# Optimization experiments

Measured on AMD Instinct MI355X. Metric: run time of the kernel, lower is better.

Reference implementation:

```python
import jax, jax.numpy as jnp
import numpy as np

G = 16  # grid (window) size, fixed in the module


def _ln_channels(x, w, b, eps=1e-5):
    # LayerNorm4D: normalize over channel dim of NCHW
    mu = x.mean(axis=1, keepdims=True)
    var = ((x - mu) ** 2).mean(axis=1, keepdims=True)
    return (x - mu) / jnp.sqrt(var + eps) * w[None, :, None, None] + b[None, :, None, None]


def setup_inputs() -> dict:
    key = jax.random.key(0)
    ks = jax.random.split(key, 8)
    B, C, H, W = 8, 256, 128, 128
    C8, F = C // 8, 4 * C
    s = 0.02
    return {
        "x": jax.random.normal(ks[0], (B, C, H, W), jnp.float32),
        "Wq": jax.random.normal(ks[1], (C8, C), jnp.float32) * s,
        "Wk": jax.random.normal(ks[2], (C8, C), jnp.float32) * s,
        "Wv": jax.random.normal(ks[3], (C, C), jnp.float32) * s,
        "gamma": jnp.float32(1.0),
        "W1": jax.random.normal(ks[4], (F, C), jnp.float32) * s,
        "b1": jnp.zeros((F,), jnp.float32),
        "W2": jax.random.normal(ks[5], (C, F), jnp.float32) * s,
        "b2": jnp.zeros((C,), jnp.float32),
        "ln1_w": jnp.ones((C,), jnp.float32),
        "ln1_b": jnp.zeros((C,), jnp.float32),
        "ln2_w": jnp.ones((C,), jnp.float32),
        "ln2_b": jnp.zeros((C,), jnp.float32),
    }


def reference(x, Wq, Wk, Wv, gamma, W1, b1, W2, b2, ln1_w, ln1_b, ln2_w, ln2_b):
    B, C, H, W = x.shape
    nh, nw = H // G, W // G
    N = G * G  # tokens per window
    # gather all 16x16 windows into the batch dim: [B*nh*nw, C, N]
    xw = x.reshape(B, C, nh, G, nw, G).transpose(0, 2, 4, 1, 3, 5).reshape(B * nh * nw, C, N)
    # SAGAN-style self-attention within each window
    q = jnp.einsum('oc,bcn->bno', Wq, xw)                 # [Bw, N, C/8]
    k = jnp.einsum('oc,bcn->bon', Wk, xw)                 # [Bw, C/8, N]
    attn = jax.nn.softmax(jnp.einsum('bno,bom->bnm', q, k), axis=-1)  # [Bw, N, N]
    v = jnp.einsum('oc,bcn->bon', Wv, xw)                 # [Bw, C, N]
    out = jnp.einsum('bcn,bmn->bcm', v, attn)             # v @ attn^T
    aw = gamma * out + xw
    # scatter windows back to NCHW
    xa = aw.reshape(B, nh, nw, C, G, G).transpose(0, 3, 1, 4, 2, 5).reshape(B, C, H, W)
    # FFN: 1x1 conv -> GELU(exact) -> 1x1 conv (dropout is identity in eval)
    h1 = jax.nn.gelu(jnp.einsum('fc,bchw->bfhw', W1, xa) + b1[None, :, None, None], approximate=False)
    y = jnp.einsum('cf,bfhw->bchw', W2, h1) + b2[None, :, None, None]
    x2 = xa + _ln_channels(y, ln1_w, ln1_b)
    return x2 + _ln_channels(x2, ln2_w, ln2_b)
```

## Files before the change

### kernel.cpp

```cpp
#include <hip/hip_runtime.h>
#include <hip/hip_bf16.h>

#define C_DIM 256
#define HW_DIM 16384
#define F_DIM 1024

typedef __hip_bfloat16 bf16;
typedef short short8 __attribute__((ext_vector_type(8)));
typedef float f32x4 __attribute__((ext_vector_type(4)));

__device__ __forceinline__ float bf2f(unsigned short u) {
  unsigned int x = ((unsigned int)u) << 16;
  return __uint_as_float(x);
}
__device__ __forceinline__ unsigned short f2bfbits(float v) {
  bf16 h = __float2bfloat16(v);
  return *(unsigned short*)&h;
}


__global__ __launch_bounds__(256) void prep_weights(
    const float* __restrict__ Wq, const float* __restrict__ Wk,
    const float* __restrict__ Wv, const float* __restrict__ W1,
    const float* __restrict__ W2, unsigned short* __restrict__ Wqkv,
    unsigned short* __restrict__ W1s, unsigned short* __restrict__ W2s) {
  int i = blockIdx.x * 256 + threadIdx.x;
  if (i < 320 * 256) {
    int r = i >> 8, c = i & 255;
    float v;
    if (r < 32)      v = Wq[r * 256 + c];
    else if (r < 64) v = Wk[(r - 32) * 256 + c];
    else             v = Wv[(r - 64) * 256 + c];
    Wqkv[i] = f2bfbits(v);
  }
  if (i < 32768) {
    int ft = i >> 9, ks = (i >> 6) & 7, l = i & 63;
    int f = ft * 16 + (l & 15), kb = ks * 32 + (l >> 4) * 8;
    #pragma unroll
    for (int j = 0; j < 8; ++j)
      W1s[i * 8 + j] = f2bfbits(W1[f * 256 + kb + j]);
  }
  if (i < 32768) {
    int ct = i >> 11, gks = (i >> 6) & 31, l = i & 63;
    int c = ct * 16 + (l & 15), fb = gks * 32 + (l >> 4) * 8;
    #pragma unroll
    for (int j = 0; j < 8; ++j)
      W2s[i * 8 + j] = f2bfbits(W2[c * 1024 + fb + j]);
  }
}

__global__ __launch_bounds__(256) void qkvx_kernel(
    const float* __restrict__ x, const unsigned short* __restrict__ Wqkv,
    unsigned short* __restrict__ Xfrag, unsigned short* __restrict__ Qw,
    unsigned short* __restrict__ Kw, unsigned short* __restrict__ Vw) {
  __shared__ __align__(16) short Xs[4][8][64][8];

  const int bid = blockIdx.x;
  const int win = bid >> 2, mc = bid & 3;
  const int b = win >> 6, wh = (win >> 3) & 7, ww = win & 7;
  const int m0 = mc * 64;
  const int tid = threadIdx.x;
  const int wv = tid >> 6, l = tid & 63;
  const int t = l & 15, q = l >> 4;

  unsigned short* XFb = Xfrag + (size_t)win * 65536 + (size_t)mc * 16384;
  short8* XsLin = (short8*)&Xs[0][0][0][0];

  #pragma unroll
  for (int rep = 0; rep < 8; ++rep) {
    const int idx = rep * 256 + tid;
    const int mt_l = idx >> 9, kss = (idx >> 6) & 7, ll = idx & 63;
    const int tt = ll & 15, qq = ll >> 4;
    const int h = wh * 16 + mc * 4 + mt_l, w = ww * 16 + tt;
    const int c0 = kss * 32 + qq * 8;
    const float* xp = x + ((size_t)(b * 256 + c0) * 128 + h) * 128 + w;
    short8 v;
    #pragma unroll
    for (int j = 0; j < 8; ++j)
      v[j] = (short)f2bfbits(xp[(size_t)j * 16384]);
    XsLin[idx] = v;
    *(short8*)(XFb + (size_t)idx * 8) = v;
  }
  __syncthreads();

  const int r0 = wv * 16;
  unsigned short* const QKdst = (wv < 2) ? Qw : Kw;
  const int o0 = (wv & 1) * 16 + q * 4;

  for (int mt = 0; mt < 4; ++mt) {
    short8 Bf[8];
    #pragma unroll
    for (int ks = 0; ks < 8; ++ks)
      Bf[ks] = *(const short8*)&Xs[mt][ks][l][0];

    {
      f32x4 acc = (f32x4){0.f, 0.f, 0.f, 0.f};
      #pragma unroll
      for (int ks = 0; ks < 8; ++ks) {
        short8 av = *(const short8*)(Wqkv + (size_t)(r0 + t) * 256 + ks * 32 + q * 8);
        acc = __builtin_amdgcn_mfma_f32_16x16x32_bf16(av, Bf[ks], acc, 0, 0, 0);
      }
      const int n = m0 + mt * 16 + t;
      ushort4 u;
      u.x = f2bfbits(acc[0]); u.y = f2bfbits(acc[1]);
      u.z = f2bfbits(acc[2]); u.w = f2bfbits(acc[3]);
      *(ushort4*)(QKdst + ((size_t)win * 256 + n) * 32 + o0) = u;
    }

    #pragma unroll
    for (int i = 0; i < 4; ++i) {
      const int c0 = (wv * 4 + i) * 16;
      f32x4 acc = (f32x4){0.f, 0.f, 0.f, 0.f};
      #pragma unroll
      for (int ks = 0; ks < 8; ++ks) {
        short8 av = *(const short8*)(Wqkv + (size_t)(64 + c0 + t) * 256 + ks * 32 + q * 8);
        acc = __builtin_amdgcn_mfma_f32_16x16x32_bf16(Bf[ks], av, acc, 0, 0, 0);
      }
      ushort4 u;
      u.x = f2bfbits(acc[0]); u.y = f2bfbits(acc[1]);
      u.z = f2bfbits(acc[2]); u.w = f2bfbits(acc[3]);
      *(ushort4*)(Vw + ((size_t)win * 256 + c0 + t) * 256 + m0 + mt * 16 + q * 4) = u;
    }
  }
}

__global__ __launch_bounds__(256, 3) void attn_ffn_kernel(
    const unsigned short* __restrict__ Qw, const unsigned short* __restrict__ Kw,
    const unsigned short* __restrict__ Vw, const unsigned short* __restrict__ Xfrag,
    const float* __restrict__ gamma,
    const unsigned short* __restrict__ W1s, const unsigned short* __restrict__ W2s,
    const float* __restrict__ b1, const float* __restrict__ b2,
    const float* __restrict__ ln1w, const float* __restrict__ ln1b,
    const float* __restrict__ ln2w, const float* __restrict__ ln2b,
    float* __restrict__ out) {
  __shared__ __align__(16) short XfPs[16384];
  __shared__ __align__(16) short Htf[4][4][64][8];
  __shared__ float red[2][4][64];
  __shared__ float Ls[64];

  short (*Ps)[64][72] = (short(*)[64][72])&XfPs[0];
  float* Lpart = (float*)&XfPs[9216];
  short (*Xf)[8][64][8] = (short(*)[8][64][8])&XfPs[0];

  const int bid = blockIdx.x;
  const int wgb = (bid & 7) * 256 + (bid >> 3);
  const int win = wgb >> 2, wr = wgb & 3;
  const int b = win >> 6, wh = (win >> 3) & 7, ww = win & 7;

  const int tid = threadIdx.x;
  const int wc = tid >> 6, l = tid & 63;
  const int t = l & 15, q = l >> 4;

  f32x4 Oacc[4][4];
  #pragma unroll
  for (int k = 0; k < 4; ++k)
    #pragma unroll
    for (int i = 0; i < 4; ++i)
      Oacc[k][i] = (f32x4){0.f, 0.f, 0.f, 0.f};
  float lsum[16];
  #pragma unroll
  for (int e = 0; e < 16; ++e) lsum[e] = 0.f;

  const unsigned short* Qb = Qw + (size_t)win * 256 * 32;
  const unsigned short* Kb = Kw + (size_t)win * 256 * 32;
  const unsigned short* Vb = Vw + (size_t)win * 65536;

  short8 aq[4];
  #pragma unroll
  for (int i = 0; i < 4; ++i)
    aq[i] = *(const short8*)(Qb + (size_t)((wr * 4 + i) * 16 + t) * 32 + q * 8);

  for (int mcc = 0; mcc < 4; ++mcc) {
    const int buf = mcc & 1;
    {
      const int m0s = (mcc * 4 + wc) * 16;
      short8 bk = *(const short8*)(Kb + (size_t)(m0s + t) * 32 + q * 8);
      f32x4 sv[4];
      #pragma unroll
      for (int i = 0; i < 4; ++i)
        sv[i] = __builtin_amdgcn_mfma_f32_16x16x32_bf16(aq[i], bk, (f32x4){0.f,0.f,0.f,0.f}, 0, 0, 0);
      #pragma unroll
      for (int i = 0; i < 4; ++i) {
        #pragma unroll
        for (int r = 0; r < 4; ++r) {
          float e = __expf(sv[i][r]);
          lsum[i * 4 + r] += e;
          Ps[buf][i * 16 + q * 4 + r][wc * 16 + t] = (short)f2bfbits(e);
        }
      }
    }
    __syncthreads();
    #pragma unroll
    for (int ks2 = 0; ks2 < 2; ++ks2) {
      short8 ap[4], bv[4];
      #pragma unroll
      for (int i = 0; i < 4; ++i)
        ap[i] = *(const short8*)&Ps[buf][i * 16 + t][ks2 * 32 + q * 8];
      #pragma unroll
      for (int k = 0; k < 4; ++k)
        bv[k] = *(const short8*)(Vb + (size_t)((wc * 4 + k) * 16 + t) * 256 + mcc * 64 + ks2 * 32 + q * 8);
      #pragma unroll
      for (int k = 0; k < 4; ++k)
        #pragma unroll
        for (int i = 0; i < 4; ++i)
          Oacc[k][i] = __builtin_amdgcn_mfma_f32_16x16x32_bf16(bv[k], ap[i], Oacc[k][i], 0, 0, 0);
    }
  }

  #pragma unroll
  for (int mask = 1; mask < 16; mask <<= 1)
    #pragma unroll
    for (int e = 0; e < 16; ++e)
      lsum[e] += __shfl_xor(lsum[e], mask);
  __syncthreads();
  if (t == 0) {
    #pragma unroll
    for (int i = 0; i < 4; ++i)
      *(float4*)&Lpart[wc * 64 + i * 16 + q * 4] =
          make_float4(lsum[i * 4 + 0], lsum[i * 4 + 1], lsum[i * 4 + 2], lsum[i * 4 + 3]);
  }
  __syncthreads();
  if (tid < 64) {
    float s = Lpart[tid] + Lpart[64 + tid] + Lpart[128 + tid] + Lpart[192 + tid];
    Ls[tid] = gamma[0] / s;
  }
  __syncthreads();

  const unsigned short* Xres = Xfrag + (size_t)win * 65536;
  #pragma unroll
  for (int i = 0; i < 4; ++i) {
    const float ls = Ls[i * 16 + t];
    #pragma unroll
    for (int k = 0; k < 4; ++k) {
      const int ksx = wc * 2 + (k >> 1);
      const int lx = ((k & 1) * 2 + (q >> 1)) * 16 + t;
      const int jx = (q & 1) * 4;
      const size_t goff = (((size_t)(wr * 4 + i) * 8 + ksx) * 64 + lx) * 8 + jx;
      ushort4 xa4 = *(const ushort4*)(Xres + goff);
      const unsigned short* xp = (const unsigned short*)&xa4;
      ushort4 u;
      unsigned short* up = (unsigned short*)&u;
      #pragma unroll
      for (int r = 0; r < 4; ++r)
        up[r] = f2bfbits(ls * Oacc[k][i][r] + bf2f(xp[r]));
      *(ushort4*)&Xf[i][ksx][lx][jx] = u;
    }
  }
  __syncthreads();

  const int p = t;
  const int wv = wc;

  f32x4 Yacc[4][4];
  #pragma unroll
  for (int i = 0; i < 4; ++i)
    #pragma unroll
    for (int pt = 0; pt < 4; ++pt)
      Yacc[i][pt] = (f32x4){0.f, 0.f, 0.f, 0.f};

  const short8* W1s8 = (const short8*)W1s;
  const short8* W2s8 = (const short8*)W2s;

  for (int fc = 0; fc < 8; ++fc) {
    f32x4 Hacc[2][4];
    #pragma unroll
    for (int i = 0; i < 2; ++i)
      #pragma unroll
      for (int pt = 0; pt < 4; ++pt)
        Hacc[i][pt] = (f32x4){0.f, 0.f, 0.f, 0.f};
    const int f0 = (fc * 8 + wv * 2) * 8;
    #pragma unroll
    for (int ks = 0; ks < 8; ++ks) {
      short8 a0 = W1s8[(f0 + ks) * 64 + l];
      short8 a1 = W1s8[(f0 + 8 + ks) * 64 + l];
      #pragma unroll
      for (int pt = 0; pt < 4; ++pt) {
        short8 bf = *(const short8*)&Xf[pt][ks][l][0];
        Hacc[0][pt] = __builtin_amdgcn_mfma_f32_16x16x32_bf16(a0, bf, Hacc[0][pt], 0, 0, 0);
        Hacc[1][pt] = __builtin_amdgcn_mfma_f32_16x16x32_bf16(a1, bf, Hacc[1][pt], 0, 0, 0);
      }
    }
    __syncthreads();
    #pragma unroll
    for (int i = 0; i < 2; ++i) {
      float4 bv1 = *(const float4*)(b1 + fc * 128 + wv * 32 + i * 16 + q * 4);
      #pragma unroll
      for (int pt = 0; pt < 4; ++pt) {
        ushort4 hbv;
        unsigned short* hp = (unsigned short*)&hbv;
        #pragma unroll
        for (int r = 0; r < 4; ++r) {
          float v = Hacc[i][pt][r] + ((const float*)&bv1)[r];
          float a = 1.5957691216f * fmaf(0.044715f * v, v * v, v);
          float e = __expf(a);
          float g = v - v * __builtin_amdgcn_rcpf(e + 1.f);
          hp[r] = f2bfbits(g);
        }
        *(ushort4*)&Htf[pt][wv][(i * 2 + (q >> 1)) * 16 + p][(q & 1) * 4] = hbv;
      }
    }
    __syncthreads();
    #pragma unroll
    for (int fs = 0; fs < 4; ++fs) {
      short8 av[4];
      #pragma unroll
      for (int i = 0; i < 4; ++i)
        av[i] = W2s8[((wv * 4 + i) * 32 + fc * 4 + fs) * 64 + l];
      #pragma unroll
      for (int pt = 0; pt < 4; ++pt) {
        short8 bf = *(const short8*)&Htf[pt][fs][l][0];
        #pragma unroll
        for (int i = 0; i < 4; ++i)
          Yacc[i][pt] = __builtin_amdgcn_mfma_f32_16x16x32_bf16(av[i], bf, Yacc[i][pt], 0, 0, 0);
      }
    }
  }

  #pragma unroll
  for (int i = 0; i < 4; ++i) {
    float4 bb = *(const float4*)(b2 + wv * 64 + i * 16 + q * 4);
    #pragma unroll
    for (int pt = 0; pt < 4; ++pt)
      #pragma unroll
      for (int r = 0; r < 4; ++r)
        Yacc[i][pt][r] += ((const float*)&bb)[r];
  }

  #pragma unroll
  for (int pt = 0; pt < 4; ++pt) {
    float ss = 0.f, sq = 0.f;
    #pragma unroll
    for (int i = 0; i < 4; ++i)
      #pragma unroll
      for (int r = 0; r < 4; ++r) { float v = Yacc[i][pt][r]; ss += v; sq += v * v; }
    ss += __shfl_xor(ss, 16); sq += __shfl_xor(sq, 16);
    ss += __shfl_xor(ss, 32); sq += __shfl_xor(sq, 32);
    if (l < 16) { red[0][wv][pt * 16 + l] = ss; red[1][wv][pt * 16 + l] = sq; }
  }
  __syncthreads();
  if (tid < 64) {
    float S  = red[0][0][tid] + red[0][1][tid] + red[0][2][tid] + red[0][3][tid];
    float Q2 = red[1][0][tid] + red[1][1][tid] + red[1][2][tid] + red[1][3][tid];
    float m = S * 0.00390625f;
    float va = Q2 * 0.00390625f - m * m;
    red[0][0][tid] = m; red[1][0][tid] = rsqrtf(va + 1e-5f);
  }
  __syncthreads();
  #pragma unroll
  for (int i = 0; i < 4; ++i) {
    float4 w1v = *(const float4*)(ln1w + wv * 64 + i * 16 + q * 4);
    float4 b1v = *(const float4*)(ln1b + wv * 64 + i * 16 + q * 4);
    const int ksx = wv * 2 + (i >> 1);
    const int lq = (i & 1) * 2 + (q >> 1);
    #pragma unroll
    for (int pt = 0; pt < 4; ++pt) {
      int px = pt * 16 + p;
      float mu = red[0][0][px], rs = red[1][0][px];
      ushort4 xa4 = *(const ushort4*)&Xf[pt][ksx][lq * 16 + p][(q & 1) * 4];
      const unsigned short* xp = (const unsigned short*)&xa4;
      #pragma unroll
      for (int r = 0; r < 4; ++r)
        Yacc[i][pt][r] = bf2f(xp[r]) + (Yacc[i][pt][r] - mu) * rs * ((const float*)&w1v)[r] + ((const float*)&b1v)[r];
    }
  }
  __syncthreads();
  #pragma unroll
  for (int pt = 0; pt < 4; ++pt) {
    float ss = 0.f, sq = 0.f;
    #pragma unroll
    for (int i = 0; i < 4; ++i)
      #pragma unroll
      for (int r = 0; r < 4; ++r) { float v = Yacc[i][pt][r]; ss += v; sq += v * v; }
    ss += __shfl_xor(ss, 16); sq += __shfl_xor(sq, 16);
    ss += __shfl_xor(ss, 32); sq += __shfl_xor(sq, 32);
    if (l < 16) { red[0][wv][pt * 16 + l] = ss; red[1][wv][pt * 16 + l] = sq; }
  }
  __syncthreads();
  if (tid < 64) {
    float S  = red[0][0][tid] + red[0][1][tid] + red[0][2][tid] + red[0][3][tid];
    float Q2 = red[1][0][tid] + red[1][1][tid] + red[1][2][tid] + red[1][3][tid];
    float m = S * 0.00390625f;
    float va = Q2 * 0.00390625f - m * m;
    red[0][0][tid] = m; red[1][0][tid] = rsqrtf(va + 1e-5f);
  }
  __syncthreads();
  #pragma unroll
  for (int i = 0; i < 4; ++i) {
    float4 w2v = *(const float4*)(ln2w + wv * 64 + i * 16 + q * 4);
    float4 b2v = *(const float4*)(ln2b + wv * 64 + i * 16 + q * 4);
    #pragma unroll
    for (int pt = 0; pt < 4; ++pt) {
      int px = pt * 16 + p;
      float mu = red[0][0][px], rs = red[1][0][px];
      #pragma unroll
      for (int r = 0; r < 4; ++r) {
        int c = wv * 64 + i * 16 + q * 4 + r;
        float x2 = Yacc[i][pt][r];
        float o = x2 + (x2 - mu) * rs * ((const float*)&w2v)[r] + ((const float*)&b2v)[r];
        out[(((size_t)(b * 256 + c) * 128) + wh * 16 + wr * 4 + pt) * 128 + ww * 16 + p] = o;
      }
    }
  }
}

extern "C" void kernel_launch(void* const* d_in, const int* in_sizes, int n_in,
                              void* d_out, int out_size, void* d_ws, size_t ws_size,
                              hipStream_t stream) {
  const float* x     = (const float*)d_in[0];
  const float* Wq    = (const float*)d_in[1];
  const float* Wk    = (const float*)d_in[2];
  const float* Wv    = (const float*)d_in[3];
  const float* gamma = (const float*)d_in[4];
  const float* W1    = (const float*)d_in[5];
  const float* b1    = (const float*)d_in[6];
  const float* W2    = (const float*)d_in[7];
  const float* b2    = (const float*)d_in[8];
  const float* ln1w  = (const float*)d_in[9];
  const float* ln1b  = (const float*)d_in[10];
  const float* ln2w  = (const float*)d_in[11];
  const float* ln2b  = (const float*)d_in[12];
  float* out = (float*)d_out;

  char* wsb = (char*)d_ws;
  unsigned short* Xfrag = (unsigned short*)wsb;
  unsigned short* Vw    = (unsigned short*)(wsb + 67108864);
  unsigned short* Qw    = (unsigned short*)(wsb + 134217728);
  unsigned short* Kw    = (unsigned short*)(wsb + 142606336);
  unsigned short* Wqkv  = (unsigned short*)(wsb + 150994944);
  unsigned short* W1s   = (unsigned short*)(wsb + 151158784);
  unsigned short* W2s   = (unsigned short*)(wsb + 151683072);

  prep_weights<<<1024, 256, 0, stream>>>(Wq, Wk, Wv, W1, W2, Wqkv, W1s, W2s);
  qkvx_kernel<<<2048, 256, 0, stream>>>(x, Wqkv, Xfrag, Qw, Kw, Vw);
  attn_ffn_kernel<<<2048, 256, 0, stream>>>(Qw, Kw, Vw, Xfrag, gamma,
                                            W1s, W2s, b1, b2, ln1w, ln1b, ln2w, ln2b, out);
}
```

Before: 580.9 us.

## Coalesce x loads, hoist QKV weights, halve FFN tile for 4 waves/SIMD

The QKV projection kernel now reads x with float4 loads that are coalesced along width and scatters them into the LDS fragment layout. Xfrag is then copied out of LDS, and the weight fragments are hoisted out of the token loop. The attention+FFN kernel splits each FFN chunk into two halves with a smaller hidden tile and aliases the Ls/red buffers into one shared array, cutting LDS use and registers so occupancy can rise from 3 to 4 workgroups. The cost is twice as many barriers in the FFN loop and a risk of register spills under the tighter launch bound.

```diff
diff --git a/kernel.cpp b/kernel.cpp
--- a/kernel.cpp
+++ b/kernel.cpp
@@ -66,39 +66,45 @@
   unsigned short* XFb = Xfrag + (size_t)win * 65536 + (size_t)mc * 16384;
   short8* XsLin = (short8*)&Xs[0][0][0][0];
 
+  {
+    const int h_l = (tid >> 2) & 3, w4 = tid & 3;
+    const int crow = tid >> 4;
+    const int h = wh * 16 + mc * 4 + h_l;
+    const float* xbase = x + ((size_t)b * 256 * 128 + h) * 128 + ww * 16 + w4 * 4;
+    #pragma unroll
+    for (int it = 0; it < 16; ++it) {
+      const int c = it * 16 + crow;
+      float4 v = *(const float4*)(xbase + (size_t)c * 16384);
+      const int ks = c >> 5, qd = (c >> 3) & 3, j = c & 7;
+      const float* vf = (const float*)&v;
+      #pragma unroll
+      for (int e = 0; e < 4; ++e)
+        Xs[h_l][ks][qd * 16 + w4 * 4 + e][j] = (short)f2bfbits(vf[e]);
+    }
+  }
+  __syncthreads();
+
   #pragma unroll
   for (int rep = 0; rep < 8; ++rep) {
-    const int idx = rep * 256 + tid;
-    const int mt_l = idx >> 9, kss = (idx >> 6) & 7, ll = idx & 63;
-    const int tt = ll & 15, qq = ll >> 4;
-    const int h = wh * 16 + mc * 4 + mt_l, w = ww * 16 + tt;
-    const int c0 = kss * 32 + qq * 8;
-    const float* xp = x + ((size_t)(b * 256 + c0) * 128 + h) * 128 + w;
-    short8 v;
-    #pragma unroll
-    for (int j = 0; j < 8; ++j)
-      v[j] = (short)f2bfbits(xp[(size_t)j * 16384]);
-    XsLin[idx] = v;
-    *(short8*)(XFb + (size_t)idx * 8) = v;
-  }
-  __syncthreads();
-
-  const int r0 = wv * 16;
-  unsigned short* const QKdst = (wv < 2) ? Qw : Kw;
-  const int o0 = (wv & 1) * 16 + q * 4;
-
-  for (int mt = 0; mt < 4; ++mt) {
-    short8 Bf[8];
+    short8 v = XsLin[rep * 256 + tid];
+    *(short8*)(XFb + ((size_t)rep * 256 + tid) * 8) = v;
+  }
+
+  {
+    const int r0 = wv * 16;
+    unsigned short* const QKdst = (wv < 2) ? Qw : Kw;
+    const int o0 = (wv & 1) * 16 + q * 4;
+    short8 avqk[8];
     #pragma unroll
     for (int ks = 0; ks < 8; ++ks)
-      Bf[ks] = *(const short8*)&Xs[mt][ks][l][0];
-
-    {
+      avqk[ks] = *(const short8*)(Wqkv + (size_t)(r0 + t) * 256 + ks * 32 + q * 8);
+    #pragma unroll
+    for (int mt = 0; mt < 4; ++mt) {
       f32x4 acc = (f32x4){0.f, 0.f, 0.f, 0.f};
       #pragma unroll
       for (int ks = 0; ks < 8; ++ks) {
-        short8 av = *(const short8*)(Wqkv + (size_t)(r0 + t) * 256 + ks * 32 + q * 8);
-        acc = __builtin_amdgcn_mfma_f32_16x16x32_bf16(av, Bf[ks], acc, 0, 0, 0);
+        short8 bf = *(const short8*)&Xs[mt][ks][l][0];
+        acc = __builtin_amdgcn_mfma_f32_16x16x32_bf16(avqk[ks], bf, acc, 0, 0, 0);
       }
       const int n = m0 + mt * 16 + t;
       ushort4 u;
@@ -106,15 +112,21 @@
       u.z = f2bfbits(acc[2]); u.w = f2bfbits(acc[3]);
       *(ushort4*)(QKdst + ((size_t)win * 256 + n) * 32 + o0) = u;
     }
-
-    #pragma unroll
-    for (int i = 0; i < 4; ++i) {
-      const int c0 = (wv * 4 + i) * 16;
+  }
+
+  for (int i = 0; i < 4; ++i) {
+    const int c0 = (wv * 4 + i) * 16;
+    short8 avv[8];
+    #pragma unroll
+    for (int ks = 0; ks < 8; ++ks)
+      avv[ks] = *(const short8*)(Wqkv + (size_t)(64 + c0 + t) * 256 + ks * 32 + q * 8);
+    #pragma unroll
+    for (int mt = 0; mt < 4; ++mt) {
       f32x4 acc = (f32x4){0.f, 0.f, 0.f, 0.f};
       #pragma unroll
       for (int ks = 0; ks < 8; ++ks) {
-        short8 av = *(const short8*)(Wqkv + (size_t)(64 + c0 + t) * 256 + ks * 32 + q * 8);
-        acc = __builtin_amdgcn_mfma_f32_16x16x32_bf16(Bf[ks], av, acc, 0, 0, 0);
+        short8 bf = *(const short8*)&Xs[mt][ks][l][0];
+        acc = __builtin_amdgcn_mfma_f32_16x16x32_bf16(bf, avv[ks], acc, 0, 0, 0);
       }
       ushort4 u;
       u.x = f2bfbits(acc[0]); u.y = f2bfbits(acc[1]);
@@ -124,7 +136,7 @@
   }
 }
 
-__global__ __launch_bounds__(256, 3) void attn_ffn_kernel(
+__global__ __launch_bounds__(256, 4) void attn_ffn_kernel(
     const unsigned short* __restrict__ Qw, const unsigned short* __restrict__ Kw,
     const unsigned short* __restrict__ Vw, const unsigned short* __restrict__ Xfrag,
     const float* __restrict__ gamma,
@@ -133,14 +145,14 @@
     const float* __restrict__ ln1w, const float* __restrict__ ln1b,
     const float* __restrict__ ln2w, const float* __restrict__ ln2b,
     float* __restrict__ out) {
-  __shared__ __align__(16) short XfPs[16384];
-  __shared__ __align__(16) short Htf[4][4][64][8];
-  __shared__ float red[2][4][64];
-  __shared__ float Ls[64];
-
-  short (*Ps)[64][72] = (short(*)[64][72])&XfPs[0];
-  float* Lpart = (float*)&XfPs[9216];
-  short (*Xf)[8][64][8] = (short(*)[8][64][8])&XfPs[0];
+  __shared__ __align__(16) short SMEM[20480];
+
+  short (*Ps)[64][72] = (short(*)[64][72])&SMEM[0];
+  float* Lpart = (float*)&SMEM[9216];
+  short (*Xf)[8][64][8] = (short(*)[8][64][8])&SMEM[0];
+  short (*Htf2)[2][64][8] = (short(*)[2][64][8])&SMEM[16384];
+  float* Ls   = (float*)&SMEM[16384];
+  float* redS = (float*)&SMEM[16384 + 128];
 
   const int bid = blockIdx.x;
   const int wgb = (bid & 7) * 256 + (bid >> 3);
@@ -262,59 +274,61 @@
   const short8* W2s8 = (const short8*)W2s;
 
   for (int fc = 0; fc < 8; ++fc) {
-    f32x4 Hacc[2][4];
-    #pragma unroll
-    for (int i = 0; i < 2; ++i)
+    #pragma unroll
+    for (int h2 = 0; h2 < 2; ++h2) {
+      f32x4 Hacc[4];
       #pragma unroll
       for (int pt = 0; pt < 4; ++pt)
-        Hacc[i][pt] = (f32x4){0.f, 0.f, 0.f, 0.f};
-    const int f0 = (fc * 8 + wv * 2) * 8;
-    #pragma unroll
-    for (int ks = 0; ks < 8; ++ks) {
-      short8 a0 = W1s8[(f0 + ks) * 64 + l];
-      short8 a1 = W1s8[(f0 + 8 + ks) * 64 + l];
-      #pragma unroll
-      for (int pt = 0; pt < 4; ++pt) {
-        short8 bf = *(const short8*)&Xf[pt][ks][l][0];
-        Hacc[0][pt] = __builtin_amdgcn_mfma_f32_16x16x32_bf16(a0, bf, Hacc[0][pt], 0, 0, 0);
-        Hacc[1][pt] = __builtin_amdgcn_mfma_f32_16x16x32_bf16(a1, bf, Hacc[1][pt], 0, 0, 0);
-      }
-    }
-    __syncthreads();
-    #pragma unroll
-    for (int i = 0; i < 2; ++i) {
-      float4 bv1 = *(const float4*)(b1 + fc * 128 + wv * 32 + i * 16 + q * 4);
-      #pragma unroll
-      for (int pt = 0; pt < 4; ++pt) {
-        ushort4 hbv;
-        unsigned short* hp = (unsigned short*)&hbv;
-        #pragma unroll
-        for (int r = 0; r < 4; ++r) {
-          float v = Hacc[i][pt][r] + ((const float*)&bv1)[r];
-          float a = 1.5957691216f * fmaf(0.044715f * v, v * v, v);
-          float e = __expf(a);
-          float g = v - v * __builtin_amdgcn_rcpf(e + 1.f);
-          hp[r] = f2bfbits(g);
+        Hacc[pt] = (f32x4){0.f, 0.f, 0.f, 0.f};
+      const int ft = fc * 8 + h2 * 4 + wv;
+      #pragma unroll
+      for (int ks = 0; ks < 8; ++ks) {
+        short8 a0 = W1s8[(ft * 8 + ks) * 64 + l];
+        #pragma unroll
+        for (int pt = 0; pt < 4; ++pt) {
+          short8 bf = *(const short8*)&Xf[pt][ks][l][0];
+          Hacc[pt] = __builtin_amdgcn_mfma_f32_16x16x32_bf16(a0, bf, Hacc[pt], 0, 0, 0);
         }
-        *(ushort4*)&Htf[pt][wv][(i * 2 + (q >> 1)) * 16 + p][(q & 1) * 4] = hbv;
-      }
-    }
-    __syncthreads();
-    #pragma unroll
-    for (int fs = 0; fs < 4; ++fs) {
-      short8 av[4];
-      #pragma unroll
-      for (int i = 0; i < 4; ++i)
-        av[i] = W2s8[((wv * 4 + i) * 32 + fc * 4 + fs) * 64 + l];
-      #pragma unroll
-      for (int pt = 0; pt < 4; ++pt) {
-        short8 bf = *(const short8*)&Htf[pt][fs][l][0];
+      }
+      __syncthreads();
+      {
+        float4 bv1 = *(const float4*)(b1 + fc * 128 + h2 * 64 + wv * 16 + q * 4);
+        const int fs2 = wv >> 1;
+        const int lq = ((wv & 1) * 2 + (q >> 1)) * 16 + p;
+        const int jx = (q & 1) * 4;
+        #pragma unroll
+        for (int pt = 0; pt < 4; ++pt) {
+          ushort4 hbv;
+          unsigned short* hp = (unsigned short*)&hbv;
+          #pragma unroll
+          for (int r = 0; r < 4; ++r) {
+            float v = Hacc[pt][r] + ((const float*)&bv1)[r];
+            float a = 1.5957691216f * fmaf(0.044715f * v, v * v, v);
+            float e = __expf(a);
+            float g = v - v * __builtin_amdgcn_rcpf(e + 1.f);
+            hp[r] = f2bfbits(g);
+          }
+          *(ushort4*)&Htf2[pt][fs2][lq][jx] = hbv;
+        }
+      }
+      __syncthreads();
+      #pragma unroll
+      for (int fs2 = 0; fs2 < 2; ++fs2) {
+        short8 av[4];
         #pragma unroll
         for (int i = 0; i < 4; ++i)
-          Yacc[i][pt] = __builtin_amdgcn_mfma_f32_16x16x32_bf16(av[i], bf, Yacc[i][pt], 0, 0, 0);
-      }
-    }
-  }
+          av[i] = W2s8[((wv * 4 + i) * 32 + fc * 4 + h2 * 2 + fs2) * 64 + l];
+        #pragma unroll
+        for (int pt = 0; pt < 4; ++pt) {
+          short8 bf = *(const short8*)&Htf2[pt][fs2][l][0];
+          #pragma unroll
+          for (int i = 0; i < 4; ++i)
+            Yacc[i][pt] = __builtin_amdgcn_mfma_f32_16x16x32_bf16(av[i], bf, Yacc[i][pt], 0, 0, 0);
+        }
+      }
+    }
+  }
+  __syncthreads();
 
   #pragma unroll
   for (int i = 0; i < 4; ++i) {
@@ -335,15 +349,15 @@
       for (int r = 0; r < 4; ++r) { float v = Yacc[i][pt][r]; ss += v; sq += v * v; }
     ss += __shfl_xor(ss, 16); sq += __shfl_xor(sq, 16);
     ss += __shfl_xor(ss, 32); sq += __shfl_xor(sq, 32);
-    if (l < 16) { red[0][wv][pt * 16 + l] = ss; red[1][wv][pt * 16 + l] = sq; }
+    if (l < 16) { redS[wv * 64 + pt * 16 + l] = ss; redS[256 + wv * 64 + pt * 16 + l] = sq; }
   }
   __syncthreads();
   if (tid < 64) {
-    float S  = red[0][0][tid] + red[0][1][tid] + red[0][2][tid] + red[0][3][tid];
-    float Q2 = red[1][0][tid] + red[1][1][tid] + red[1][2][tid] + red[1][3][tid];
+    float S  = redS[tid] + redS[64 + tid] + redS[128 + tid] + redS[192 + tid];
+    float Q2 = redS[256 + tid] + redS[320 + tid] + redS[384 + tid] + redS[448 + tid];
     float m = S * 0.00390625f;
     float va = Q2 * 0.00390625f - m * m;
-    red[0][0][tid] = m; red[1][0][tid] = rsqrtf(va + 1e-5f);
+    redS[tid] = m; redS[256 + tid] = rsqrtf(va + 1e-5f);
   }
   __syncthreads();
   #pragma unroll
@@ -355,7 +369,7 @@
     #pragma unroll
     for (int pt = 0; pt < 4; ++pt) {
       int px = pt * 16 + p;
-      float mu = red[0][0][px], rs = red[1][0][px];
+      float mu = redS[px], rs = redS[256 + px];
       ushort4 xa4 = *(const ushort4*)&Xf[pt][ksx][lq * 16 + p][(q & 1) * 4];
       const unsigned short* xp = (const unsigned short*)&xa4;
       #pragma unroll
@@ -373,15 +387,15 @@
       for (int r = 0; r < 4; ++r) { float v = Yacc[i][pt][r]; ss += v; sq += v * v; }
     ss += __shfl_xor(ss, 16); sq += __shfl_xor(sq, 16);
     ss += __shfl_xor(ss, 32); sq += __shfl_xor(sq, 32);
-    if (l < 16) { red[0][wv][pt * 16 + l] = ss; red[1][wv][pt * 16 + l] = sq; }
+    if (l < 16) { redS[wv * 64 + pt * 16 + l] = ss; redS[256 + wv * 64 + pt * 16 + l] = sq; }
   }
   __syncthreads();
   if (tid < 64) {
-    float S  = red[0][0][tid] + red[0][1][tid] + red[0][2][tid] + red[0][3][tid];
-    float Q2 = red[1][0][tid] + red[1][1][tid] + red[1][2][tid] + red[1][3][tid];
+    float S  = redS[tid] + redS[64 + tid] + redS[128 + tid] + redS[192 + tid];
+    float Q2 = redS[256 + tid] + redS[320 + tid] + redS[384 + tid] + redS[448 + tid];
     float m = S * 0.00390625f;
     float va = Q2 * 0.00390625f - m * m;
-    red[0][0][tid] = m; red[1][0][tid] = rsqrtf(va + 1e-5f);
+    redS[tid] = m; redS[256 + tid] = rsqrtf(va + 1e-5f);
   }
   __syncthreads();
   #pragma unroll
@@ -391,7 +405,7 @@
     #pragma unroll
     for (int pt = 0; pt < 4; ++pt) {
       int px = pt * 16 + p;
-      float mu = red[0][0][px], rs = red[1][0][px];
+      float mu = redS[px], rs = redS[256 + px];
       #pragma unroll
       for (int r = 0; r < 4; ++r) {
         int c = wv * 64 + i * 16 + q * 4 + r;
```

After: 727.0 us. 1.25x slower.

## Coalesce x loads, hoist weight fragments, and prefetch V and residual tiles

Applied to the files above, without the earlier changes.

The qkvx kernel now loads x as float4 along the width dimension and transposes it into the shared-memory fragment layout, instead of issuing eight strided scalar loads per fragment. It then writes Xfrag from shared memory. The QK and V projections are reordered so each weight fragment is loaded once from global memory and reused across the four m-tiles, while X fragments are re-read from LDS. In the attention kernel, V fragments are software-prefetched one chunk ahead and the residual Xfrag values are loaded before the softmax-sum reduction. This hides global latency at the cost of more registers, which may reduce occupancy at the launch bounds of 3 blocks per SM.

```diff
diff --git a/kernel.cpp b/kernel.cpp
--- a/kernel.cpp
+++ b/kernel.cpp
@@ -66,39 +66,45 @@
   unsigned short* XFb = Xfrag + (size_t)win * 65536 + (size_t)mc * 16384;
   short8* XsLin = (short8*)&Xs[0][0][0][0];
 
+  {
+    const int h_l = (tid >> 2) & 3, w4 = tid & 3;
+    const int crow = tid >> 4;
+    const int h = wh * 16 + mc * 4 + h_l;
+    const float* xbase = x + ((size_t)b * 256 * 128 + h) * 128 + ww * 16 + w4 * 4;
+    #pragma unroll
+    for (int it = 0; it < 16; ++it) {
+      const int c = it * 16 + crow;
+      float4 v = *(const float4*)(xbase + (size_t)c * 16384);
+      const int ks = c >> 5, qd = (c >> 3) & 3, j = c & 7;
+      const float* vf = (const float*)&v;
+      #pragma unroll
+      for (int e = 0; e < 4; ++e)
+        Xs[h_l][ks][qd * 16 + w4 * 4 + e][j] = (short)f2bfbits(vf[e]);
+    }
+  }
+  __syncthreads();
+
   #pragma unroll
   for (int rep = 0; rep < 8; ++rep) {
-    const int idx = rep * 256 + tid;
-    const int mt_l = idx >> 9, kss = (idx >> 6) & 7, ll = idx & 63;
-    const int tt = ll & 15, qq = ll >> 4;
-    const int h = wh * 16 + mc * 4 + mt_l, w = ww * 16 + tt;
-    const int c0 = kss * 32 + qq * 8;
-    const float* xp = x + ((size_t)(b * 256 + c0) * 128 + h) * 128 + w;
-    short8 v;
-    #pragma unroll
-    for (int j = 0; j < 8; ++j)
-      v[j] = (short)f2bfbits(xp[(size_t)j * 16384]);
-    XsLin[idx] = v;
-    *(short8*)(XFb + (size_t)idx * 8) = v;
-  }
-  __syncthreads();
-
-  const int r0 = wv * 16;
-  unsigned short* const QKdst = (wv < 2) ? Qw : Kw;
-  const int o0 = (wv & 1) * 16 + q * 4;
-
-  for (int mt = 0; mt < 4; ++mt) {
-    short8 Bf[8];
+    short8 v = XsLin[rep * 256 + tid];
+    *(short8*)(XFb + ((size_t)rep * 256 + tid) * 8) = v;
+  }
+
+  {
+    const int r0 = wv * 16;
+    unsigned short* const QKdst = (wv < 2) ? Qw : Kw;
+    const int o0 = (wv & 1) * 16 + q * 4;
+    short8 avqk[8];
     #pragma unroll
     for (int ks = 0; ks < 8; ++ks)
-      Bf[ks] = *(const short8*)&Xs[mt][ks][l][0];
-
-    {
+      avqk[ks] = *(const short8*)(Wqkv + (size_t)(r0 + t) * 256 + ks * 32 + q * 8);
+    #pragma unroll
+    for (int mt = 0; mt < 4; ++mt) {
       f32x4 acc = (f32x4){0.f, 0.f, 0.f, 0.f};
       #pragma unroll
       for (int ks = 0; ks < 8; ++ks) {
-        short8 av = *(const short8*)(Wqkv + (size_t)(r0 + t) * 256 + ks * 32 + q * 8);
-        acc = __builtin_amdgcn_mfma_f32_16x16x32_bf16(av, Bf[ks], acc, 0, 0, 0);
+        short8 bf = *(const short8*)&Xs[mt][ks][l][0];
+        acc = __builtin_amdgcn_mfma_f32_16x16x32_bf16(avqk[ks], bf, acc, 0, 0, 0);
       }
       const int n = m0 + mt * 16 + t;
       ushort4 u;
@@ -106,15 +112,21 @@
       u.z = f2bfbits(acc[2]); u.w = f2bfbits(acc[3]);
       *(ushort4*)(QKdst + ((size_t)win * 256 + n) * 32 + o0) = u;
     }
-
-    #pragma unroll
-    for (int i = 0; i < 4; ++i) {
-      const int c0 = (wv * 4 + i) * 16;
+  }
+
+  for (int i = 0; i < 4; ++i) {
+    const int c0 = (wv * 4 + i) * 16;
+    short8 avv[8];
+    #pragma unroll
+    for (int ks = 0; ks < 8; ++ks)
+      avv[ks] = *(const short8*)(Wqkv + (size_t)(64 + c0 + t) * 256 + ks * 32 + q * 8);
+    #pragma unroll
+    for (int mt = 0; mt < 4; ++mt) {
       f32x4 acc = (f32x4){0.f, 0.f, 0.f, 0.f};
       #pragma unroll
       for (int ks = 0; ks < 8; ++ks) {
-        short8 av = *(const short8*)(Wqkv + (size_t)(64 + c0 + t) * 256 + ks * 32 + q * 8);
-        acc = __builtin_amdgcn_mfma_f32_16x16x32_bf16(Bf[ks], av, acc, 0, 0, 0);
+        short8 bf = *(const short8*)&Xs[mt][ks][l][0];
+        acc = __builtin_amdgcn_mfma_f32_16x16x32_bf16(bf, avv[ks], acc, 0, 0, 0);
       }
       ushort4 u;
       u.x = f2bfbits(acc[0]); u.y = f2bfbits(acc[1]);
@@ -170,6 +182,14 @@
   for (int i = 0; i < 4; ++i)
     aq[i] = *(const short8*)(Qb + (size_t)((wr * 4 + i) * 16 + t) * 32 + q * 8);
 
+  short8 bvp[2][4];
+  #pragma unroll
+  for (int ks2 = 0; ks2 < 2; ++ks2)
+    #pragma unroll
+    for (int k = 0; k < 4; ++k)
+      bvp[ks2][k] = *(const short8*)(Vb + (size_t)((wc * 4 + k) * 16 + t) * 256 + ks2 * 32 + q * 8);
+
+  #pragma unroll
   for (int mcc = 0; mcc < 4; ++mcc) {
     const int buf = mcc & 1;
     {
@@ -189,55 +209,78 @@
         }
       }
     }
+    short8 bvn[2][4];
+    if (mcc < 3) {
+      #pragma unroll
+      for (int ks2 = 0; ks2 < 2; ++ks2)
+        #pragma unroll
+        for (int k = 0; k < 4; ++k)
+          bvn[ks2][k] = *(const short8*)(Vb + (size_t)((wc * 4 + k) * 16 + t) * 256 + (mcc + 1) * 64 + ks2 * 32 + q * 8);
+    }
     __syncthreads();
     #pragma unroll
     for (int ks2 = 0; ks2 < 2; ++ks2) {
-      short8 ap[4], bv[4];
+      short8 ap[4];
       #pragma unroll
       for (int i = 0; i < 4; ++i)
         ap[i] = *(const short8*)&Ps[buf][i * 16 + t][ks2 * 32 + q * 8];
       #pragma unroll
       for (int k = 0; k < 4; ++k)
-        bv[k] = *(const short8*)(Vb + (size_t)((wc * 4 + k) * 16 + t) * 256 + mcc * 64 + ks2 * 32 + q * 8);
-      #pragma unroll
-      for (int k = 0; k < 4; ++k)
         #pragma unroll
         for (int i = 0; i < 4; ++i)
-          Oacc[k][i] = __builtin_amdgcn_mfma_f32_16x16x32_bf16(bv[k], ap[i], Oacc[k][i], 0, 0, 0);
-    }
-  }
-
-  #pragma unroll
-  for (int mask = 1; mask < 16; mask <<= 1)
-    #pragma unroll
-    for (int e = 0; e < 16; ++e)
-      lsum[e] += __shfl_xor(lsum[e], mask);
-  __syncthreads();
-  if (t == 0) {
-    #pragma unroll
-    for (int i = 0; i < 4; ++i)
-      *(float4*)&Lpart[wc * 64 + i * 16 + q * 4] =
-          make_float4(lsum[i * 4 + 0], lsum[i * 4 + 1], lsum[i * 4 + 2], lsum[i * 4 + 3]);
-  }
-  __syncthreads();
-  if (tid < 64) {
-    float s = Lpart[tid] + Lpart[64 + tid] + Lpart[128 + tid] + Lpart[192 + tid];
-    Ls[tid] = gamma[0] / s;
-  }
-  __syncthreads();
+          Oacc[k][i] = __builtin_amdgcn_mfma_f32_16x16x32_bf16(bvp[ks2][k], ap[i], Oacc[k][i], 0, 0, 0);
+    }
+    if (mcc < 3) {
+      #pragma unroll
+      for (int ks2 = 0; ks2 < 2; ++ks2)
+        #pragma unroll
+        for (int k = 0; k < 4; ++k)
+          bvp[ks2][k] = bvn[ks2][k];
+    }
+  }
 
   const unsigned short* Xres = Xfrag + (size_t)win * 65536;
-  #pragma unroll
-  for (int i = 0; i < 4; ++i) {
-    const float ls = Ls[i * 16 + t];
+  ushort4 xres_pre[4][4];
+  #pragma unroll
+  for (int i = 0; i < 4; ++i) {
     #pragma unroll
     for (int k = 0; k < 4; ++k) {
       const int ksx = wc * 2 + (k >> 1);
       const int lx = ((k & 1) * 2 + (q >> 1)) * 16 + t;
       const int jx = (q & 1) * 4;
       const size_t goff = (((size_t)(wr * 4 + i) * 8 + ksx) * 64 + lx) * 8 + jx;
-      ushort4 xa4 = *(const ushort4*)(Xres + goff);
-      const unsigned short* xp = (const unsigned short*)&xa4;
+      xres_pre[i][k] = *(const ushort4*)(Xres + goff);
+    }
+  }
+
+  #pragma unroll
+  for (int mask = 1; mask < 16; mask <<= 1)
+    #pragma unroll
+    for (int e = 0; e < 16; ++e)
+      lsum[e] += __shfl_xor(lsum[e], mask);
+  __syncthreads();
+  if (t == 0) {
+    #pragma unroll
+    for (int i = 0; i < 4; ++i)
+      *(float4*)&Lpart[wc * 64 + i * 16 + q * 4] =
+          make_float4(lsum[i * 4 + 0], lsum[i * 4 + 1], lsum[i * 4 + 2], lsum[i * 4 + 3]);
+  }
+  __syncthreads();
+  if (tid < 64) {
+    float s = Lpart[tid] + Lpart[64 + tid] + Lpart[128 + tid] + Lpart[192 + tid];
+    Ls[tid] = gamma[0] / s;
+  }
+  __syncthreads();
+
+  #pragma unroll
+  for (int i = 0; i < 4; ++i) {
+    const float ls = Ls[i * 16 + t];
+    #pragma unroll
+    for (int k = 0; k < 4; ++k) {
+      const int ksx = wc * 2 + (k >> 1);
+      const int lx = ((k & 1) * 2 + (q >> 1)) * 16 + t;
+      const int jx = (q & 1) * 4;
+      const unsigned short* xp = (const unsigned short*)&xres_pre[i][k];
       ushort4 u;
       unsigned short* up = (unsigned short*)&u;
       #pragma unroll
```

Measured after the change: 589.3 us. Within noise of the previous version (+1.4%).
